# Kernel optimization log

Measured on AMD Instinct MI355X. Metric: run time of the kernel, lower is better.

The kernel has to match this reference:

```python
import jax, jax.numpy as jnp
import numpy as np

D_MODEL = 1024
D_STATE = 128


def setup_inputs() -> dict:
    key = jax.random.key(0)
    ks = jax.random.split(key, 16)
    dm, ds = D_MODEL, D_STATE
    def lin(kw, kb, out_f, in_f):
        # torch nn.Linear default init: U(-1/sqrt(in), 1/sqrt(in))
        bound = 1.0 / np.sqrt(in_f)
        W = jax.random.uniform(kw, (out_f, in_f), jnp.float32, -bound, bound)
        b = jax.random.uniform(kb, (out_f,), jnp.float32, -bound, bound)
        return W, b
    x = jax.random.normal(ks[0], (8, 2048, dm), jnp.float32)
    A = jax.random.normal(ks[1], (ds, ds), jnp.float32) * 0.05  # scaled for stability of the recurrence
    B_w, B_b = lin(ks[2], ks[3], ds, dm)
    C_w, C_b = lin(ks[4], ks[5], dm, ds)
    D_w, D_b = lin(ks[6], ks[7], dm, dm)
    s_w1, s_b1 = lin(ks[8], ks[9], dm // 2, dm)
    s_w2, s_b2 = lin(ks[10], ks[11], ds, dm // 2)
    g_w, g_b = lin(ks[12], ks[13], dm, dm)
    return {"x": x, "A": A, "B_w": B_w, "B_b": B_b, "C_w": C_w, "C_b": C_b,
            "D_w": D_w, "D_b": D_b, "s_w1": s_w1, "s_b1": s_b1,
            "s_w2": s_w2, "s_b2": s_b2, "g_w": g_w, "g_b": g_b}


def reference(x, A, B_w, B_b, C_w, C_b, D_w, D_b, s_w1, s_b1, s_w2, s_b2, g_w, g_b):
    # Precompute all per-timestep input projections as batched GEMMs.
    s = jax.nn.sigmoid(jax.nn.silu(jnp.einsum('btd,hd->bth', x, s_w1) + s_b1)
                       @ s_w2.T + s_b2)            # [B,T,d_state] selection gate
    Bt = jnp.einsum('btd,sd->bts', x, B_w) + B_b    # [B,T,d_state]
    u = Bt * s                                      # driving input to the recurrence

    # Linear recurrence h_t = h_{t-1} @ A.T + u_t via lax.scan over time.
    h0 = jnp.zeros((x.shape[0], A.shape[0]), x.dtype)
    def step(h, u_t):
        h = h @ A.T + u_t
        return h, h
    _, hs = jax.lax.scan(step, h0, jnp.swapaxes(u, 0, 1))  # [T,B,d_state]
    hs = jnp.swapaxes(hs, 0, 1)                            # [B,T,d_state]

    y = jnp.einsum('bts,ds->btd', hs, C_w) + C_b + jnp.einsum('btd,ed->bte', x, D_w) + D_b
    gate = jax.nn.sigmoid(jnp.einsum('btd,ed->bte', x, g_w) + g_b)
    return y * gate
```

## Files before the change

### kernel.cpp

```cpp
#include <hip/hip_runtime.h>
#include <hip/hip_bf16.h>

typedef __bf16 bf16x8 __attribute__((ext_vector_type(8)));
typedef float f32x4 __attribute__((ext_vector_type(4)));

#define M_TOK 16384
#define CHUNK 64
#define NCHUNK 32

__device__ __forceinline__ void gload16(const void* g, void* l) {
    __builtin_amdgcn_global_load_lds(
        (const __attribute__((address_space(1))) void*)g,
        (__attribute__((address_space(3))) void*)l, 16, 0, 0);
}

__device__ __forceinline__ float sigmoidf_(float v) { return 1.f / (1.f + __expf(-v)); }

__global__ __launch_bounds__(256) void f32_to_bf16_k(const float* __restrict__ in,
                                                     __hip_bfloat16* __restrict__ out, int n8) {
    int i = blockIdx.x * 256 + threadIdx.x;
    if (i >= n8) return;
    const f32x4* p4 = reinterpret_cast<const f32x4*>(in) + (size_t)i * 2;
    f32x4 a = p4[0], b = p4[1];
    union { __hip_bfloat16 h[8]; uint4 u; } o;
    o.h[0] = __float2bfloat16(a[0]); o.h[1] = __float2bfloat16(a[1]);
    o.h[2] = __float2bfloat16(a[2]); o.h[3] = __float2bfloat16(a[3]);
    o.h[4] = __float2bfloat16(b[0]); o.h[5] = __float2bfloat16(b[1]);
    o.h[6] = __float2bfloat16(b[2]); o.h[7] = __float2bfloat16(b[3]);
    *reinterpret_cast<uint4*>(out + (size_t)i * 8) = o.u;
}

__global__ __launch_bounds__(256)
void wconv6(const float* s0, const float* s1, const float* s2, const float* s3,
            const float* s4, const float* s5,
            __hip_bfloat16* d0, __hip_bfloat16* d1, __hip_bfloat16* d2,
            __hip_bfloat16* d3, __hip_bfloat16* d4, __hip_bfloat16* d5,
            int n0, int n1, int n2, int n3, int n4, int n5) {
    const float* src; __hip_bfloat16* dst; int n8;
    switch (blockIdx.y) {
        case 0: src = s0; dst = d0; n8 = n0; break;
        case 1: src = s1; dst = d1; n8 = n1; break;
        case 2: src = s2; dst = d2; n8 = n2; break;
        case 3: src = s3; dst = d3; n8 = n3; break;
        case 4: src = s4; dst = d4; n8 = n4; break;
        default: src = s5; dst = d5; n8 = n5; break;
    }
    int i = blockIdx.x * 256 + threadIdx.x;
    if (i >= n8) return;
    const f32x4* p4 = reinterpret_cast<const f32x4*>(src) + (size_t)i * 2;
    f32x4 a = p4[0], b = p4[1];
    union { __hip_bfloat16 h[8]; uint4 u; } o;
    o.h[0] = __float2bfloat16(a[0]); o.h[1] = __float2bfloat16(a[1]);
    o.h[2] = __float2bfloat16(a[2]); o.h[3] = __float2bfloat16(a[3]);
    o.h[4] = __float2bfloat16(b[0]); o.h[5] = __float2bfloat16(b[1]);
    o.h[6] = __float2bfloat16(b[2]); o.h[7] = __float2bfloat16(b[3]);
    *reinterpret_cast<uint4*>(dst + (size_t)i * 8) = o.u;
}

__device__ __forceinline__ void stage128(const __hip_bfloat16* src, int ldk, size_t row0,
                                         int k0, char* lds, int tid) {
    #pragma unroll
    for (int j = 0; j < 4; ++j) {
        int q = tid + 256 * j;
        int row = q >> 3, c8 = q & 7;
        int cb = (c8 * 16) ^ ((row & 7) << 4);
        gload16((const char*)(src + (row0 + row) * (size_t)ldk + k0) + cb, lds + q * 16);
    }
}

template<int MODE>
__global__ __launch_bounds__(256, 2)
void gemm128(const __hip_bfloat16* __restrict__ X, const __hip_bfloat16* __restrict__ W,
             const __hip_bfloat16* __restrict__ Gw, const __hip_bfloat16* __restrict__ HS,
             const __hip_bfloat16* __restrict__ CW,
             const float* __restrict__ bias, const float* __restrict__ bias2,
             const float* __restrict__ biasG,
             float* __restrict__ outF, __hip_bfloat16* __restrict__ outB) {
    constexpr int N = (MODE == 0) ? 512 : 1024;
    constexpr int nN = N / 128;
    __shared__ __align__(16) char Xs[16384];
    __shared__ __align__(16) char Ws[16384];
    __shared__ __align__(16) char Gs[(MODE == 1) ? 16384 : 16];

    const int nwg  = gridDim.x;
    const int orig = blockIdx.x;
    const int v    = (orig & 7) * (nwg >> 3) + (orig >> 3);
    const size_t m0 = (size_t)(v / nN) * 128;
    const int    n0 = (v % nN) * 128;
    const int tid = threadIdx.x, lane = tid & 63, wid = tid >> 6;
    const int wm = wid >> 1, wn = wid & 1;
    const int lr = lane & 15, lg = lane >> 4;

    auto frag = [&](const char* base, int R, int kk) -> bf16x8 {
        int cb = (kk * 64 + lg * 16) ^ ((R & 7) << 4);
        return *reinterpret_cast<const bf16x8*>(base + R * 128 + cb);
    };

    f32x4 accY[4][4] = {};
    f32x4 accG[(MODE == 1) ? 4 : 1][4] = {};

    for (int k0 = 0; k0 < 1024; k0 += 64) {
        __syncthreads();
        stage128(X, 1024, m0, k0, Xs, tid);
        stage128(W, 1024, (size_t)n0, k0, Ws, tid);
        if constexpr (MODE == 1) stage128(Gw, 1024, (size_t)n0, k0, Gs, tid);
        __syncthreads();
        #pragma unroll
        for (int kk = 0; kk < 2; ++kk) {
            bf16x8 af[4];
            #pragma unroll
            for (int m = 0; m < 4; ++m) af[m] = frag(Xs, wm*64 + m*16 + lr, kk);
            #pragma unroll
            for (int n = 0; n < 4; ++n) {
                bf16x8 bw = frag(Ws, wn*64 + n*16 + lr, kk);
                #pragma unroll
                for (int m = 0; m < 4; ++m)
                    accY[m][n] = __builtin_amdgcn_mfma_f32_16x16x32_bf16(af[m], bw, accY[m][n], 0, 0, 0);
                if constexpr (MODE == 1) {
                    bf16x8 bg = frag(Gs, wn*64 + n*16 + lr, kk);
                    #pragma unroll
                    for (int m = 0; m < 4; ++m)
                        accG[m][n] = __builtin_amdgcn_mfma_f32_16x16x32_bf16(af[m], bg, accG[m][n], 0, 0, 0);
                }
            }
        }
    }
    if constexpr (MODE == 1) {
        for (int k0 = 0; k0 < 128; k0 += 64) {
            __syncthreads();
            stage128(HS, 128, m0, k0, Xs, tid);
            stage128(CW, 128, (size_t)n0, k0, Ws, tid);
            __syncthreads();
            #pragma unroll
            for (int kk = 0; kk < 2; ++kk) {
                bf16x8 af[4];
                #pragma unroll
                for (int m = 0; m < 4; ++m) af[m] = frag(Xs, wm*64 + m*16 + lr, kk);
                #pragma unroll
                for (int n = 0; n < 4; ++n) {
                    bf16x8 bw = frag(Ws, wn*64 + n*16 + lr, kk);
                    #pragma unroll
                    for (int m = 0; m < 4; ++m)
                        accY[m][n] = __builtin_amdgcn_mfma_f32_16x16x32_bf16(af[m], bw, accY[m][n], 0, 0, 0);
                }
            }
        }
    }

    #pragma unroll
    for (int m = 0; m < 4; ++m)
        #pragma unroll
        for (int n = 0; n < 4; ++n)
            #pragma unroll
            for (int rr = 0; rr < 4; ++rr) {
                size_t row = m0 + wm*64 + m*16 + lg*4 + rr;
                int col = n0 + wn*64 + n*16 + lr;
                if constexpr (MODE == 0) {
                    float vv = accY[m][n][rr] + bias[col];
                    outB[row * N + col] = __float2bfloat16(vv * sigmoidf_(vv));
                } else {
                    float y = accY[m][n][rr] + bias[col] + bias2[col];
                    float g = accG[m][n][rr] + biasG[col];
                    outF[row * 1024 + col] = y * sigmoidf_(g);
                }
            }
}

__global__ __launch_bounds__(256)
void gemm_u(const __hip_bfloat16* __restrict__ Z1, const __hip_bfloat16* __restrict__ W2,
            const float* __restrict__ b2,
            const __hip_bfloat16* __restrict__ X, const __hip_bfloat16* __restrict__ Bw,
            const float* __restrict__ Bb, __hip_bfloat16* __restrict__ U) {
    __shared__ __align__(16) char As[64 * 128];
    __shared__ __align__(16) char Bs[128 * 128];
    const int orig = blockIdx.x;
    const int v = (orig & 7) * 32 + (orig >> 3);
    const int m0 = v * 64;
    const int tid = threadIdx.x;
    const int wid = tid >> 6, lane = tid & 63;
    const int wm = wid >> 1, wn = wid & 1;
    const int lr = lane & 15, lg = lane >> 4;
    const int srow = tid >> 3, sc8 = tid & 7;

    auto fragA = [&](int R, int kk) -> bf16x8 {
        int cb = (kk * 64 + lg * 16) ^ ((R & 7) << 4);
        return *reinterpret_cast<const bf16x8*>(As + R * 128 + cb);
    };
    auto fragB = [&](int R, int kk) -> bf16x8 {
        int cb = (kk * 64 + lg * 16) ^ ((R & 7) << 4);
        return *reinterpret_cast<const bf16x8*>(Bs + R * 128 + cb);
    };

    f32x4 accS[2][4] = {};
    for (int k0 = 0; k0 < 512; k0 += 64) {
        __syncthreads();
        #pragma unroll
        for (int j = 0; j < 2; ++j) {
            int row = srow + j * 32, q = tid + 256 * j;
            int cb = (sc8 * 16) ^ ((row & 7) << 4);
            gload16((const char*)&Z1[(size_t)(m0 + row) * 512 + k0] + cb, As + q * 16);
        }
        #pragma unroll
        for (int j = 0; j < 4; ++j) {
            int row = srow + j * 32, q = tid + 256 * j;
            int cb = (sc8 * 16) ^ ((row & 7) << 4);
            gload16((const char*)&W2[(size_t)row * 512 + k0] + cb, Bs + q * 16);
        }
        __syncthreads();
        #pragma unroll
        for (int kk = 0; kk < 2; ++kk) {
            bf16x8 af[2], bfr[4];
            #pragma unroll
            for (int m = 0; m < 2; ++m) af[m] = fragA(wm*32 + m*16 + lr, kk);
            #pragma unroll
            for (int n = 0; n < 4; ++n) bfr[n] = fragB(wn*64 + n*16 + lr, kk);
            #pragma unroll
            for (int m = 0; m < 2; ++m)
                #pragma unroll
                for (int n = 0; n < 4; ++n)
                    accS[m][n] = __builtin_amdgcn_mfma_f32_16x16x32_bf16(af[m], bfr[n], accS[m][n], 0, 0, 0);
        }
    }
    #pragma unroll
    for (int m = 0; m < 2; ++m)
        #pragma unroll
        for (int n = 0; n < 4; ++n)
            #pragma unroll
            for (int r = 0; r < 4; ++r) {
                int col = wn*64 + n*16 + lr;
                accS[m][n][r] = sigmoidf_(accS[m][n][r] + b2[col]);
            }
    f32x4 accU[2][4] = {};
    for (int k0 = 0; k0 < 1024; k0 += 64) {
        __syncthreads();
        #pragma unroll
        for (int j = 0; j < 2; ++j) {
            int row = srow + j * 32, q = tid + 256 * j;
            int cb = (sc8 * 16) ^ ((row & 7) << 4);
            gload16((const char*)&X[(size_t)(m0 + row) * 1024 + k0] + cb, As + q * 16);
        }
        #pragma unroll
        for (int j = 0; j < 4; ++j) {
            int row = srow + j * 32, q = tid + 256 * j;
            int cb = (sc8 * 16) ^ ((row & 7) << 4);
            gload16((const char*)&Bw[(size_t)row * 1024 + k0] + cb, Bs + q * 16);
        }
        __syncthreads();
        #pragma unroll
        for (int kk = 0; kk < 2; ++kk) {
            bf16x8 af[2], bfr[4];
            #pragma unroll
            for (int m = 0; m < 2; ++m) af[m] = fragA(wm*32 + m*16 + lr, kk);
            #pragma unroll
            for (int n = 0; n < 4; ++n) bfr[n] = fragB(wn*64 + n*16 + lr, kk);
            #pragma unroll
            for (int m = 0; m < 2; ++m)
                #pragma unroll
                for (int n = 0; n < 4; ++n)
                    accU[m][n] = __builtin_amdgcn_mfma_f32_16x16x32_bf16(af[m], bfr[n], accU[m][n], 0, 0, 0);
        }
    }
    #pragma unroll
    for (int m = 0; m < 2; ++m)
        #pragma unroll
        for (int n = 0; n < 4; ++n)
            #pragma unroll
            for (int r = 0; r < 4; ++r) {
                int row = m0 + wm*32 + m*16 + lg*4 + r;
                int col = wn*64 + n*16 + lr;
                float uval = (accU[m][n][r] + Bb[col]) * accS[m][n][r];
                U[(size_t)row * 128 + col] = __float2bfloat16(uval);
            }
}

__global__ __launch_bounds__(128, 1) void matpow8(const float* __restrict__ P,
                                                  float* __restrict__ O) {
    __shared__ __align__(16) float v[2][128];
    const int tid = threadIdx.x, col = blockIdx.x;
    f32x4 pr[32];
    #pragma unroll
    for (int k = 0; k < 32; ++k) pr[k] = *reinterpret_cast<const f32x4*>(&P[tid * 128 + k * 4]);
    v[0][tid] = P[tid * 128 + col];
    __syncthreads();
    int cur = 0;
    for (int it = 0; it < 7; ++it) {
        const f32x4* hv = reinterpret_cast<const f32x4*>(v[cur]);
        f32x4 s0{}, s1{}, s2{}, s3{};
        #pragma unroll
        for (int k = 0; k < 32; k += 4) {
            s0 += pr[k]     * hv[k];
            s1 += pr[k + 1] * hv[k + 1];
            s2 += pr[k + 2] * hv[k + 2];
            s3 += pr[k + 3] * hv[k + 3];
        }
        f32x4 ss = (s0 + s1) + (s2 + s3);
        v[cur ^ 1][tid] = ss[0] + ss[1] + ss[2] + ss[3];
        __syncthreads();
        cur ^= 1;
    }
    O[tid * 128 + col] = v[cur][tid];
}

__global__ __launch_bounds__(128, 1) void ssm_phase1(const float* __restrict__ A,
                                                     const __hip_bfloat16* __restrict__ u,
                                                     float* __restrict__ E) {
    __shared__ __align__(16) float hb[2][128];
    __shared__ __align__(16) __hip_bfloat16 uL[CHUNK * 128];
    const int tid = threadIdx.x;
    f32x4 ar[32];
    #pragma unroll
    for (int k = 0; k < 32; ++k) ar[k] = *reinterpret_cast<const f32x4*>(&A[tid * 128 + k * 4]);
    const int b = blockIdx.x >> 5, c = blockIdx.x & 31;
    const __hip_bfloat16* up = u + ((size_t)b * 2048 + c * CHUNK) * 128;
    #pragma unroll
    for (int q = 0; q < 8; ++q)
        gload16(up + ((size_t)(q * 128 + tid)) * 8, &uL[(q * 128 + tid) * 8]);
    hb[0][tid] = 0.f;
    __syncthreads();
    int cur = 0;
    for (int t = 0; t < CHUNK; ++t) {
        const f32x4* hv = reinterpret_cast<const f32x4*>(hb[cur]);
        f32x4 s0{}, s1{}, s2{}, s3{};
        #pragma unroll
        for (int k = 0; k < 32; k += 4) {
            s0 += ar[k]     * hv[k];
            s1 += ar[k + 1] * hv[k + 1];
            s2 += ar[k + 2] * hv[k + 2];
            s3 += ar[k + 3] * hv[k + 3];
        }
        f32x4 ss = (s0 + s1) + (s2 + s3);
        float val = ss[0] + ss[1] + ss[2] + ss[3] + __bfloat162float(uL[t * 128 + tid]);
        hb[cur ^ 1][tid] = val;
        __syncthreads();
        cur ^= 1;
    }
    E[(size_t)blockIdx.x * 128 + tid] = hb[cur][tid];
}

__global__ __launch_bounds__(128, 1) void ssm_phase2(const float* __restrict__ A64,
                                                     const float* __restrict__ E,
                                                     float* __restrict__ starts) {
    __shared__ __align__(16) float st[2][128];
    __shared__ __align__(16) float El[NCHUNK * 128];
    const int tid = threadIdx.x, b = blockIdx.x;
    f32x4 ar[32];
    #pragma unroll
    for (int k = 0; k < 32; ++k) ar[k] = *reinterpret_cast<const f32x4*>(&A64[tid * 128 + k * 4]);
    const f32x4* Eg = reinterpret_cast<const f32x4*>(E + (size_t)b * NCHUNK * 128);
    #pragma unroll
    for (int q = 0; q < 8; ++q)
        reinterpret_cast<f32x4*>(El)[q * 128 + tid] = Eg[q * 128 + tid];
    st[0][tid] = 0.f;
    __syncthreads();
    int cur = 0;
    for (int c = 0; c < NCHUNK; ++c) {
        starts[((size_t)b * NCHUNK + c) * 128 + tid] = st[cur][tid];
        const f32x4* hv = reinterpret_cast<const f32x4*>(st[cur]);
        f32x4 s0{}, s1{}, s2{}, s3{};
        #pragma unroll
        for (int k = 0; k < 32; k += 4) {
            s0 += ar[k]     * hv[k];
            s1 += ar[k + 1] * hv[k + 1];
            s2 += ar[k + 2] * hv[k + 2];
            s3 += ar[k + 3] * hv[k + 3];
        }
        f32x4 ss = (s0 + s1) + (s2 + s3);
        float val = ss[0] + ss[1] + ss[2] + ss[3] + El[c * 128 + tid];
        st[cur ^ 1][tid] = val;
        __syncthreads();
        cur ^= 1;
    }
}

__global__ __launch_bounds__(128, 1) void ssm_phase3(const float* __restrict__ A,
                                                     const __hip_bfloat16* __restrict__ u,
                                                     const float* __restrict__ starts,
                                                     __hip_bfloat16* __restrict__ hs) {
    __shared__ __align__(16) float hb[2][128];
    __shared__ __align__(16) __hip_bfloat16 uL[CHUNK * 128];
    const int tid = threadIdx.x;
    f32x4 ar[32];
    #pragma unroll
    for (int k = 0; k < 32; ++k) ar[k] = *reinterpret_cast<const f32x4*>(&A[tid * 128 + k * 4]);
    const int b = blockIdx.x >> 5, c = blockIdx.x & 31;
    const size_t tok0 = (size_t)b * 2048 + c * CHUNK;
    const __hip_bfloat16* up = u + tok0 * 128;
    #pragma unroll
    for (int q = 0; q < 8; ++q)
        gload16(up + ((size_t)(q * 128 + tid)) * 8, &uL[(q * 128 + tid) * 8]);
    hb[0][tid] = starts[(size_t)blockIdx.x * 128 + tid];
    __syncthreads();
    int cur = 0;
    for (int t = 0; t < CHUNK; ++t) {
        const f32x4* hv = reinterpret_cast<const f32x4*>(hb[cur]);
        f32x4 s0{}, s1{}, s2{}, s3{};
        #pragma unroll
        for (int k = 0; k < 32; k += 4) {
            s0 += ar[k]     * hv[k];
            s1 += ar[k + 1] * hv[k + 1];
            s2 += ar[k + 2] * hv[k + 2];
            s3 += ar[k + 3] * hv[k + 3];
        }
        f32x4 ss = (s0 + s1) + (s2 + s3);
        float val = ss[0] + ss[1] + ss[2] + ss[3] + __bfloat162float(uL[t * 128 + tid]);
        hs[(tok0 + t) * 128 + tid] = __float2bfloat16(val);
        hb[cur ^ 1][tid] = val;
        __syncthreads();
        cur ^= 1;
    }
}

extern "C" void kernel_launch(void* const* d_in, const int* in_sizes, int n_in,
                              void* d_out, int out_size, void* d_ws, size_t ws_size,
                              hipStream_t stream) {
    const float* x    = (const float*)d_in[0];
    const float* A    = (const float*)d_in[1];
    const float* B_w  = (const float*)d_in[2];
    const float* B_b  = (const float*)d_in[3];
    const float* C_w  = (const float*)d_in[4];
    const float* C_b  = (const float*)d_in[5];
    const float* D_w  = (const float*)d_in[6];
    const float* D_b  = (const float*)d_in[7];
    const float* s_w1 = (const float*)d_in[8];
    const float* s_b1 = (const float*)d_in[9];
    const float* s_w2 = (const float*)d_in[10];
    const float* s_b2 = (const float*)d_in[11];
    const float* g_w  = (const float*)d_in[12];
    const float* g_b  = (const float*)d_in[13];
    float* out = (float*)d_out;

    char* p = (char*)d_ws;
    auto alloc = [&](size_t n) { char* r = p; p += (n + 255) & ~(size_t)255; return r; };
    __hip_bfloat16* xb    = (__hip_bfloat16*)alloc((size_t)M_TOK * 1024 * 2);
    __hip_bfloat16* w1b   = (__hip_bfloat16*)alloc(512 * 1024 * 2);
    __hip_bfloat16* w2b   = (__hip_bfloat16*)alloc(128 * 512 * 2);
    __hip_bfloat16* Bwb   = (__hip_bfloat16*)alloc(128 * 1024 * 2);
    __hip_bfloat16* Cwb   = (__hip_bfloat16*)alloc(1024 * 128 * 2);
    __hip_bfloat16* Dwb   = (__hip_bfloat16*)alloc(1024 * 1024 * 2);
    __hip_bfloat16* gwb   = (__hip_bfloat16*)alloc(1024 * 1024 * 2);
    __hip_bfloat16* z1b   = (__hip_bfloat16*)alloc((size_t)M_TOK * 512 * 2);
    __hip_bfloat16* ub    = (__hip_bfloat16*)alloc((size_t)M_TOK * 128 * 2);
    __hip_bfloat16* hsb   = (__hip_bfloat16*)alloc((size_t)M_TOK * 128 * 2);
    float* pa       = (float*)alloc(128 * 128 * 4);
    float* pb       = (float*)alloc(128 * 128 * 4);
    float* Ebuf     = (float*)alloc(256 * 128 * 4);
    float* startbuf = (float*)alloc(256 * 128 * 4);

    matpow8<<<128, 128, 0, stream>>>(A,  pa);
    matpow8<<<128, 128, 0, stream>>>(pa, pb);

    f32_to_bf16_k<<<dim3((M_TOK * 1024 / 8 + 255) / 256), dim3(256), 0, stream>>>(
        x, xb, M_TOK * 1024 / 8);
    wconv6<<<dim3(512, 6), dim3(256), 0, stream>>>(
        s_w1, s_w2, B_w, C_w, D_w, g_w,
        w1b, w2b, Bwb, Cwb, Dwb, gwb,
        512 * 1024 / 8, 128 * 512 / 8, 128 * 1024 / 8, 1024 * 128 / 8,
        1024 * 1024 / 8, 1024 * 1024 / 8);

    gemm128<0><<<dim3(512), dim3(256), 0, stream>>>(
        xb, w1b, nullptr, nullptr, nullptr, s_b1, nullptr, nullptr, nullptr, z1b);
    gemm_u<<<dim3(256), dim3(256), 0, stream>>>(z1b, w2b, s_b2, xb, Bwb, B_b, ub);

    ssm_phase1<<<256, 128, 0, stream>>>(A, ub, Ebuf);
    ssm_phase2<<<8, 128, 0, stream>>>(pb, Ebuf, startbuf);
    ssm_phase3<<<256, 128, 0, stream>>>(A, ub, startbuf, hsb);

    gemm128<1><<<dim3(1024), dim3(256), 0, stream>>>(
        xb, Dwb, gwb, hsb, Cwb, D_b, C_b, g_b, out, nullptr);
}
```

Before: 229.4 us.

## Split SSM scan dot products across two thread halves, merge conversions, precompute load pointers

The three SSM recurrence kernels now use 256 threads per block. Each state row's 128-wide dot product is split between two threads and combined through shared memory, which shortens the serial per-step latency but adds a second barrier per timestep. The activation and weight fp32-to-bf16 conversions are merged into one launch with a flat block-range dispatch. The GEMM staging loops now precompute global and LDS addresses once and advance pointers instead of recomputing swizzled offsets every k-step.

```diff
diff --git a/kernel.cpp b/kernel.cpp
--- a/kernel.cpp
+++ b/kernel.cpp
@@ -16,56 +16,30 @@
 
 __device__ __forceinline__ float sigmoidf_(float v) { return 1.f / (1.f + __expf(-v)); }
 
-__global__ __launch_bounds__(256) void f32_to_bf16_k(const float* __restrict__ in,
-                                                     __hip_bfloat16* __restrict__ out, int n8) {
-    int i = blockIdx.x * 256 + threadIdx.x;
-    if (i >= n8) return;
-    const f32x4* p4 = reinterpret_cast<const f32x4*>(in) + (size_t)i * 2;
+__global__ __launch_bounds__(256)
+void convall(const float* s0, const float* s1, const float* s2, const float* s3,
+             const float* s4, const float* s5, const float* s6,
+             __hip_bfloat16* d0, __hip_bfloat16* d1, __hip_bfloat16* d2,
+             __hip_bfloat16* d3, __hip_bfloat16* d4, __hip_bfloat16* d5,
+             __hip_bfloat16* d6) {
+    const int bid = blockIdx.x;
+    const float* s; __hip_bfloat16* d; int base;
+    if      (bid < 8192) { s = s0; d = d0; base = 0;    }
+    else if (bid < 8448) { s = s1; d = d1; base = 8192; }
+    else if (bid < 8480) { s = s2; d = d2; base = 8448; }
+    else if (bid < 8544) { s = s3; d = d3; base = 8480; }
+    else if (bid < 8608) { s = s4; d = d4; base = 8544; }
+    else if (bid < 9120) { s = s5; d = d5; base = 8608; }
+    else                 { s = s6; d = d6; base = 9120; }
+    size_t i = (size_t)(bid - base) * 256 + threadIdx.x;
+    const f32x4* p4 = reinterpret_cast<const f32x4*>(s) + i * 2;
     f32x4 a = p4[0], b = p4[1];
     union { __hip_bfloat16 h[8]; uint4 u; } o;
     o.h[0] = __float2bfloat16(a[0]); o.h[1] = __float2bfloat16(a[1]);
     o.h[2] = __float2bfloat16(a[2]); o.h[3] = __float2bfloat16(a[3]);
     o.h[4] = __float2bfloat16(b[0]); o.h[5] = __float2bfloat16(b[1]);
     o.h[6] = __float2bfloat16(b[2]); o.h[7] = __float2bfloat16(b[3]);
-    *reinterpret_cast<uint4*>(out + (size_t)i * 8) = o.u;
-}
-
-__global__ __launch_bounds__(256)
-void wconv6(const float* s0, const float* s1, const float* s2, const float* s3,
-            const float* s4, const float* s5,
-            __hip_bfloat16* d0, __hip_bfloat16* d1, __hip_bfloat16* d2,
-            __hip_bfloat16* d3, __hip_bfloat16* d4, __hip_bfloat16* d5,
-            int n0, int n1, int n2, int n3, int n4, int n5) {
-    const float* src; __hip_bfloat16* dst; int n8;
-    switch (blockIdx.y) {
-        case 0: src = s0; dst = d0; n8 = n0; break;
-        case 1: src = s1; dst = d1; n8 = n1; break;
-        case 2: src = s2; dst = d2; n8 = n2; break;
-        case 3: src = s3; dst = d3; n8 = n3; break;
-        case 4: src = s4; dst = d4; n8 = n4; break;
-        default: src = s5; dst = d5; n8 = n5; break;
-    }
-    int i = blockIdx.x * 256 + threadIdx.x;
-    if (i >= n8) return;
-    const f32x4* p4 = reinterpret_cast<const f32x4*>(src) + (size_t)i * 2;
-    f32x4 a = p4[0], b = p4[1];
-    union { __hip_bfloat16 h[8]; uint4 u; } o;
-    o.h[0] = __float2bfloat16(a[0]); o.h[1] = __float2bfloat16(a[1]);
-    o.h[2] = __float2bfloat16(a[2]); o.h[3] = __float2bfloat16(a[3]);
-    o.h[4] = __float2bfloat16(b[0]); o.h[5] = __float2bfloat16(b[1]);
-    o.h[6] = __float2bfloat16(b[2]); o.h[7] = __float2bfloat16(b[3]);
-    *reinterpret_cast<uint4*>(dst + (size_t)i * 8) = o.u;
-}
-
-__device__ __forceinline__ void stage128(const __hip_bfloat16* src, int ldk, size_t row0,
-                                         int k0, char* lds, int tid) {
-    #pragma unroll
-    for (int j = 0; j < 4; ++j) {
-        int q = tid + 256 * j;
-        int row = q >> 3, c8 = q & 7;
-        int cb = (c8 * 16) ^ ((row & 7) << 4);
-        gload16((const char*)(src + (row0 + row) * (size_t)ldk + k0) + cb, lds + q * 16);
-    }
+    *reinterpret_cast<uint4*>(d + i * 8) = o.u;
 }
 
 template<int MODE>
@@ -96,14 +70,34 @@
         return *reinterpret_cast<const bf16x8*>(base + R * 128 + cb);
     };
 
+    const char* gx[4]; const char* gw[4]; const char* gg[4];
+    char* lx[4]; char* lw[4]; char* lg_[4];
+    int rowq[4], cbq[4];
+    #pragma unroll
+    for (int j = 0; j < 4; ++j) {
+        int q = tid + 256 * j;
+        rowq[j] = q >> 3;
+        cbq[j] = ((q & 7) * 16) ^ ((rowq[j] & 7) << 4);
+        gx[j] = (const char*)(X + (m0 + rowq[j]) * (size_t)1024) + cbq[j];
+        gw[j] = (const char*)(W + ((size_t)(n0 + rowq[j])) * 1024) + cbq[j];
+        if constexpr (MODE == 1)
+            gg[j] = (const char*)(Gw + ((size_t)(n0 + rowq[j])) * 1024) + cbq[j];
+        lx[j] = Xs + q * 16; lw[j] = Ws + q * 16; lg_[j] = Gs + q * 16;
+    }
+
     f32x4 accY[4][4] = {};
     f32x4 accG[(MODE == 1) ? 4 : 1][4] = {};
 
     for (int k0 = 0; k0 < 1024; k0 += 64) {
         __syncthreads();
-        stage128(X, 1024, m0, k0, Xs, tid);
-        stage128(W, 1024, (size_t)n0, k0, Ws, tid);
-        if constexpr (MODE == 1) stage128(Gw, 1024, (size_t)n0, k0, Gs, tid);
+        #pragma unroll
+        for (int j = 0; j < 4; ++j) { gload16(gx[j], lx[j]); gx[j] += 128; }
+        #pragma unroll
+        for (int j = 0; j < 4; ++j) { gload16(gw[j], lw[j]); gw[j] += 128; }
+        if constexpr (MODE == 1) {
+            #pragma unroll
+            for (int j = 0; j < 4; ++j) { gload16(gg[j], lg_[j]); gg[j] += 128; }
+        }
         __syncthreads();
         #pragma unroll
         for (int kk = 0; kk < 2; ++kk) {
@@ -126,10 +120,17 @@
         }
     }
     if constexpr (MODE == 1) {
+        #pragma unroll
+        for (int j = 0; j < 4; ++j) {
+            gx[j] = (const char*)(HS + (m0 + rowq[j]) * (size_t)128) + cbq[j];
+            gw[j] = (const char*)(CW + ((size_t)(n0 + rowq[j])) * 128) + cbq[j];
+        }
         for (int k0 = 0; k0 < 128; k0 += 64) {
             __syncthreads();
-            stage128(HS, 128, m0, k0, Xs, tid);
-            stage128(CW, 128, (size_t)n0, k0, Ws, tid);
+            #pragma unroll
+            for (int j = 0; j < 4; ++j) { gload16(gx[j], lx[j]); gx[j] += 128; }
+            #pragma unroll
+            for (int j = 0; j < 4; ++j) { gload16(gw[j], lw[j]); gw[j] += 128; }
             __syncthreads();
             #pragma unroll
             for (int kk = 0; kk < 2; ++kk) {
@@ -180,7 +181,6 @@
     const int wid = tid >> 6, lane = tid & 63;
     const int wm = wid >> 1, wn = wid & 1;
     const int lr = lane & 15, lg = lane >> 4;
-    const int srow = tid >> 3, sc8 = tid & 7;
 
     auto fragA = [&](int R, int kk) -> bf16x8 {
         int cb = (kk * 64 + lg * 16) ^ ((R & 7) << 4);
@@ -191,21 +191,34 @@
         return *reinterpret_cast<const bf16x8*>(Bs + R * 128 + cb);
     };
 
+    int rowA[2], cbA[2], rowB[4], cbB[4];
+    char* lA[2]; char* lB[4];
+    #pragma unroll
+    for (int j = 0; j < 2; ++j) {
+        int q = tid + 256 * j;
+        rowA[j] = q >> 3; cbA[j] = ((q & 7) * 16) ^ ((rowA[j] & 7) << 4);
+        lA[j] = As + q * 16;
+    }
+    #pragma unroll
+    for (int j = 0; j < 4; ++j) {
+        int q = tid + 256 * j;
+        rowB[j] = q >> 3; cbB[j] = ((q & 7) * 16) ^ ((rowB[j] & 7) << 4);
+        lB[j] = Bs + q * 16;
+    }
+
+    const char* ga[2]; const char* gb[4];
+    #pragma unroll
+    for (int j = 0; j < 2; ++j) ga[j] = (const char*)(Z1 + (size_t)(m0 + rowA[j]) * 512) + cbA[j];
+    #pragma unroll
+    for (int j = 0; j < 4; ++j) gb[j] = (const char*)(W2 + (size_t)rowB[j] * 512) + cbB[j];
+
     f32x4 accS[2][4] = {};
     for (int k0 = 0; k0 < 512; k0 += 64) {
         __syncthreads();
         #pragma unroll
-        for (int j = 0; j < 2; ++j) {
-            int row = srow + j * 32, q = tid + 256 * j;
-            int cb = (sc8 * 16) ^ ((row & 7) << 4);
-            gload16((const char*)&Z1[(size_t)(m0 + row) * 512 + k0] + cb, As + q * 16);
-        }
-        #pragma unroll
-        for (int j = 0; j < 4; ++j) {
-            int row = srow + j * 32, q = tid + 256 * j;
-            int cb = (sc8 * 16) ^ ((row & 7) << 4);
-            gload16((const char*)&W2[(size_t)row * 512 + k0] + cb, Bs + q * 16);
-        }
+        for (int j = 0; j < 2; ++j) { gload16(ga[j], lA[j]); ga[j] += 128; }
+        #pragma unroll
+        for (int j = 0; j < 4; ++j) { gload16(gb[j], lB[j]); gb[j] += 128; }
         __syncthreads();
         #pragma unroll
         for (int kk = 0; kk < 2; ++kk) {
@@ -230,21 +243,17 @@
                 int col = wn*64 + n*16 + lr;
                 accS[m][n][r] = sigmoidf_(accS[m][n][r] + b2[col]);
             }
+    #pragma unroll
+    for (int j = 0; j < 2; ++j) ga[j] = (const char*)(X + (size_t)(m0 + rowA[j]) * 1024) + cbA[j];
+    #pragma unroll
+    for (int j = 0; j < 4; ++j) gb[j] = (const char*)(Bw + (size_t)rowB[j] * 1024) + cbB[j];
     f32x4 accU[2][4] = {};
     for (int k0 = 0; k0 < 1024; k0 += 64) {
         __syncthreads();
         #pragma unroll
-        for (int j = 0; j < 2; ++j) {
-            int row = srow + j * 32, q = tid + 256 * j;
-            int cb = (sc8 * 16) ^ ((row & 7) << 4);
-            gload16((const char*)&X[(size_t)(m0 + row) * 1024 + k0] + cb, As + q * 16);
-        }
-        #pragma unroll
-        for (int j = 0; j < 4; ++j) {
-            int row = srow + j * 32, q = tid + 256 * j;
-            int cb = (sc8 * 16) ^ ((row & 7) << 4);
-            gload16((const char*)&Bw[(size_t)row * 1024 + k0] + cb, Bs + q * 16);
-        }
+        for (int j = 0; j < 2; ++j) { gload16(ga[j], lA[j]); ga[j] += 128; }
+        #pragma unroll
+        for (int j = 0; j < 4; ++j) { gload16(gb[j], lB[j]); gb[j] += 128; }
         __syncthreads();
         #pragma unroll
         for (int kk = 0; kk < 2; ++kk) {
@@ -301,110 +310,127 @@
     O[tid * 128 + col] = v[cur][tid];
 }
 
-__global__ __launch_bounds__(128, 1) void ssm_phase1(const float* __restrict__ A,
+__global__ __launch_bounds__(256, 1) void ssm_phase1(const float* __restrict__ A,
                                                      const __hip_bfloat16* __restrict__ u,
                                                      float* __restrict__ E) {
     __shared__ __align__(16) float hb[2][128];
+    __shared__ __align__(16) float ps[128];
     __shared__ __align__(16) __hip_bfloat16 uL[CHUNK * 128];
-    const int tid = threadIdx.x;
-    f32x4 ar[32];
-    #pragma unroll
-    for (int k = 0; k < 32; ++k) ar[k] = *reinterpret_cast<const f32x4*>(&A[tid * 128 + k * 4]);
+    const int tid = threadIdx.x, row = tid & 127, half = tid >> 7;
+    f32x4 ar[16];
+    #pragma unroll
+    for (int k = 0; k < 16; ++k)
+        ar[k] = *reinterpret_cast<const f32x4*>(&A[row * 128 + half * 64 + k * 4]);
     const int b = blockIdx.x >> 5, c = blockIdx.x & 31;
     const __hip_bfloat16* up = u + ((size_t)b * 2048 + c * CHUNK) * 128;
     #pragma unroll
-    for (int q = 0; q < 8; ++q)
-        gload16(up + ((size_t)(q * 128 + tid)) * 8, &uL[(q * 128 + tid) * 8]);
-    hb[0][tid] = 0.f;
+    for (int q = 0; q < 4; ++q)
+        gload16(up + ((size_t)(q * 256 + tid)) * 8, &uL[(q * 256 + tid) * 8]);
+    if (half == 0) hb[0][row] = 0.f;
     __syncthreads();
     int cur = 0;
     for (int t = 0; t < CHUNK; ++t) {
-        const f32x4* hv = reinterpret_cast<const f32x4*>(hb[cur]);
+        const f32x4* hv = reinterpret_cast<const f32x4*>(hb[cur]) + half * 16;
         f32x4 s0{}, s1{}, s2{}, s3{};
         #pragma unroll
-        for (int k = 0; k < 32; k += 4) {
+        for (int k = 0; k < 16; k += 4) {
             s0 += ar[k]     * hv[k];
             s1 += ar[k + 1] * hv[k + 1];
             s2 += ar[k + 2] * hv[k + 2];
             s3 += ar[k + 3] * hv[k + 3];
         }
         f32x4 ss = (s0 + s1) + (s2 + s3);
-        float val = ss[0] + ss[1] + ss[2] + ss[3] + __bfloat162float(uL[t * 128 + tid]);
-        hb[cur ^ 1][tid] = val;
+        float partial = ss[0] + ss[1] + ss[2] + ss[3];
+        if (half) ps[row] = partial;
+        __syncthreads();
+        if (!half)
+            hb[cur ^ 1][row] = partial + ps[row] + __bfloat162float(uL[t * 128 + row]);
         __syncthreads();
         cur ^= 1;
     }
-    E[(size_t)blockIdx.x * 128 + tid] = hb[cur][tid];
-}
-
-__global__ __launch_bounds__(128, 1) void ssm_phase2(const float* __restrict__ A64,
+    if (!half) E[(size_t)blockIdx.x * 128 + row] = hb[cur][row];
+}
+
+__global__ __launch_bounds__(256, 1) void ssm_phase2(const float* __restrict__ A64,
                                                      const float* __restrict__ E,
                                                      float* __restrict__ starts) {
     __shared__ __align__(16) float st[2][128];
+    __shared__ __align__(16) float ps[128];
     __shared__ __align__(16) float El[NCHUNK * 128];
-    const int tid = threadIdx.x, b = blockIdx.x;
-    f32x4 ar[32];
-    #pragma unroll
-    for (int k = 0; k < 32; ++k) ar[k] = *reinterpret_cast<const f32x4*>(&A64[tid * 128 + k * 4]);
+    const int tid = threadIdx.x, row = tid & 127, half = tid >> 7;
+    const int b = blockIdx.x;
+    f32x4 ar[16];
+    #pragma unroll
+    for (int k = 0; k < 16; ++k)
+        ar[k] = *reinterpret_cast<const f32x4*>(&A64[row * 128 + half * 64 + k * 4]);
     const f32x4* Eg = reinterpret_cast<const f32x4*>(E + (size_t)b * NCHUNK * 128);
     #pragma unroll
-    for (int q = 0; q < 8; ++q)
-        reinterpret_cast<f32x4*>(El)[q * 128 + tid] = Eg[q * 128 + tid];
-    st[0][tid] = 0.f;
+    for (int q = 0; q < 4; ++q)
+        reinterpret_cast<f32x4*>(El)[q * 256 + tid] = Eg[q * 256 + tid];
+    if (half == 0) st[0][row] = 0.f;
     __syncthreads();
     int cur = 0;
     for (int c = 0; c < NCHUNK; ++c) {
-        starts[((size_t)b * NCHUNK + c) * 128 + tid] = st[cur][tid];
-        const f32x4* hv = reinterpret_cast<const f32x4*>(st[cur]);
+        if (!half) starts[((size_t)b * NCHUNK + c) * 128 + row] = st[cur][row];
+        const f32x4* hv = reinterpret_cast<const f32x4*>(st[cur]) + half * 16;
         f32x4 s0{}, s1{}, s2{}, s3{};
         #pragma unroll
-        for (int k = 0; k < 32; k += 4) {
+        for (int k = 0; k < 16; k += 4) {
             s0 += ar[k]     * hv[k];
             s1 += ar[k + 1] * hv[k + 1];
             s2 += ar[k + 2] * hv[k + 2];
             s3 += ar[k + 3] * hv[k + 3];
         }
         f32x4 ss = (s0 + s1) + (s2 + s3);
-        float val = ss[0] + ss[1] + ss[2] + ss[3] + El[c * 128 + tid];
-        st[cur ^ 1][tid] = val;
+        float partial = ss[0] + ss[1] + ss[2] + ss[3];
+        if (half) ps[row] = partial;
+        __syncthreads();
+        if (!half) st[cur ^ 1][row] = partial + ps[row] + El[c * 128 + row];
         __syncthreads();
         cur ^= 1;
     }
 }
 
-__global__ __launch_bounds__(128, 1) void ssm_phase3(const float* __restrict__ A,
+__global__ __launch_bounds__(256, 1) void ssm_phase3(const float* __restrict__ A,
                                                      const __hip_bfloat16* __restrict__ u,
                                                      const float* __restrict__ starts,
                                                      __hip_bfloat16* __restrict__ hs) {
     __shared__ __align__(16) float hb[2][128];
+    __shared__ __align__(16) float ps[128];
     __shared__ __align__(16) __hip_bfloat16 uL[CHUNK * 128];
-    const int tid = threadIdx.x;
-    f32x4 ar[32];
-    #pragma unroll
-    for (int k = 0; k < 32; ++k) ar[k] = *reinterpret_cast<const f32x4*>(&A[tid * 128 + k * 4]);
+    const int tid = threadIdx.x, row = tid & 127, half = tid >> 7;
+    f32x4 ar[16];
+    #pragma unroll
+    for (int k = 0; k < 16; ++k)
+        ar[k] = *reinterpret_cast<const f32x4*>(&A[row * 128 + half * 64 + k * 4]);
     const int b = blockIdx.x >> 5, c = blockIdx.x & 31;
     const size_t tok0 = (size_t)b * 2048 + c * CHUNK;
     const __hip_bfloat16* up = u + tok0 * 128;
     #pragma unroll
-    for (int q = 0; q < 8; ++q)
-        gload16(up + ((size_t)(q * 128 + tid)) * 8, &uL[(q * 128 + tid) * 8]);
-    hb[0][tid] = starts[(size_t)blockIdx.x * 128 + tid];
+    for (int q = 0; q < 4; ++q)
+        gload16(up + ((size_t)(q * 256 + tid)) * 8, &uL[(q * 256 + tid) * 8]);
+    if (half == 0) hb[0][row] = starts[(size_t)blockIdx.x * 128 + row];
     __syncthreads();
     int cur = 0;
     for (int t = 0; t < CHUNK; ++t) {
-        const f32x4* hv = reinterpret_cast<const f32x4*>(hb[cur]);
+        const f32x4* hv = reinterpret_cast<const f32x4*>(hb[cur]) + half * 16;
         f32x4 s0{}, s1{}, s2{}, s3{};
         #pragma unroll
-        for (int k = 0; k < 32; k += 4) {
+        for (int k = 0; k < 16; k += 4) {
             s0 += ar[k]     * hv[k];
             s1 += ar[k + 1] * hv[k + 1];
             s2 += ar[k + 2] * hv[k + 2];
             s3 += ar[k + 3] * hv[k + 3];
         }
         f32x4 ss = (s0 + s1) + (s2 + s3);
-        float val = ss[0] + ss[1] + ss[2] + ss[3] + __bfloat162float(uL[t * 128 + tid]);
-        hs[(tok0 + t) * 128 + tid] = __float2bfloat16(val);
-        hb[cur ^ 1][tid] = val;
+        float partial = ss[0] + ss[1] + ss[2] + ss[3];
+        if (half) ps[row] = partial;
+        __syncthreads();
+        if (!half) {
+            float val = partial + ps[row] + __bfloat162float(uL[t * 128 + row]);
+            hs[(tok0 + t) * 128 + row] = __float2bfloat16(val);
+            hb[cur ^ 1][row] = val;
+        }
         __syncthreads();
         cur ^= 1;
     }
@@ -449,21 +475,17 @@
     matpow8<<<128, 128, 0, stream>>>(A,  pa);
     matpow8<<<128, 128, 0, stream>>>(pa, pb);
 
-    f32_to_bf16_k<<<dim3((M_TOK * 1024 / 8 + 255) / 256), dim3(256), 0, stream>>>(
-        x, xb, M_TOK * 1024 / 8);
-    wconv6<<<dim3(512, 6), dim3(256), 0, stream>>>(
-        s_w1, s_w2, B_w, C_w, D_w, g_w,
-        w1b, w2b, Bwb, Cwb, Dwb, gwb,
-        512 * 1024 / 8, 128 * 512 / 8, 128 * 1024 / 8, 1024 * 128 / 8,
-        1024 * 1024 / 8, 1024 * 1024 / 8);
+    convall<<<dim3(9632), dim3(256), 0, stream>>>(
+        x, s_w1, s_w2, B_w, C_w, D_w, g_w,
+        xb, w1b, w2b, Bwb, Cwb, Dwb, gwb);
 
     gemm128<0><<<dim3(512), dim3(256), 0, stream>>>(
         xb, w1b, nullptr, nullptr, nullptr, s_b1, nullptr, nullptr, nullptr, z1b);
     gemm_u<<<dim3(256), dim3(256), 0, stream>>>(z1b, w2b, s_b2, xb, Bwb, B_b, ub);
 
-    ssm_phase1<<<256, 128, 0, stream>>>(A, ub, Ebuf);
-    ssm_phase2<<<8, 128, 0, stream>>>(pb, Ebuf, startbuf);
-    ssm_phase3<<<256, 128, 0, stream>>>(A, ub, startbuf, hsb);
+    ssm_phase1<<<256, 256, 0, stream>>>(A, ub, Ebuf);
+    ssm_phase2<<<8, 256, 0, stream>>>(pb, Ebuf, startbuf);
+    ssm_phase3<<<256, 256, 0, stream>>>(A, ub, startbuf, hsb);
 
     gemm128<1><<<dim3(1024), dim3(256), 0, stream>>>(
         xb, Dwb, gwb, hsb, Cwb, D_b, C_b, g_b, out, nullptr);
```

Result: slower. 257.9 us (+12.4%).
